# Optimization experiments

Measured on AMD Instinct MI355X. Metric: run time of the kernel, lower is better.

Reference implementation:

```python
import jax, jax.numpy as jnp
import numpy as np

GROUPS = 32
EPS = 1e-5
NUM_HEADS = 16


def group_norm(x, gamma, beta):
    # x: [b, c, s]; GroupNorm over (c//G, s) per group, affine per channel
    b, c, s = x.shape
    xg = x.reshape(b, GROUPS, (c // GROUPS) * s)
    mean = xg.mean(axis=-1, keepdims=True)
    var = xg.var(axis=-1, keepdims=True)
    xn = ((xg - mean) * jax.lax.rsqrt(var + EPS)).reshape(b, c, s)
    return xn * gamma[None, :, None] + beta[None, :, None]


def setup_inputs() -> dict:
    key = jax.random.key(0)
    ks = jax.random.split(key, 8)
    b, c, H, W = 16, 1024, 32, 32
    ctx_dim, Sk = 2048, 256
    x = jax.random.normal(ks[0], (b, c, H, W), jnp.float32)
    context = jax.random.normal(ks[1], (b, Sk, ctx_dim), jnp.float32)
    mask = jax.random.randint(ks[2], (b, Sk), 0, 2, jnp.int32)
    gamma_x = jnp.ones((c,), jnp.float32)
    beta_x = jnp.zeros((c,), jnp.float32)
    gamma_c = jnp.ones((ctx_dim,), jnp.float32)
    beta_c = jnp.zeros((ctx_dim,), jnp.float32)
    Wq = jax.random.normal(ks[3], (c, c), jnp.float32) * (1.0 / np.sqrt(c))
    bq = jnp.zeros((c,), jnp.float32)
    Wkv = jax.random.normal(ks[4], (2 * c, ctx_dim), jnp.float32) * (1.0 / np.sqrt(ctx_dim))
    bkv = jnp.zeros((2 * c,), jnp.float32)
    # proj_out is zero-initialized in the original (zero_module); use small random
    # weights so the attention path contributes to the output / gradients.
    Wp = jax.random.normal(ks[5], (c, c), jnp.float32) * (0.02 / np.sqrt(c))
    bp = jnp.zeros((c,), jnp.float32)
    return {"x": x, "context": context, "mask": mask,
            "gamma_x": gamma_x, "beta_x": beta_x, "gamma_c": gamma_c, "beta_c": beta_c,
            "Wq": Wq, "bq": bq, "Wkv": Wkv, "bkv": bkv, "Wp": Wp, "bp": bp}


def reference(x, context, mask, gamma_x, beta_x, gamma_c, beta_c, Wq, bq, Wkv, bkv, Wp, bp):
    b, c = x.shape[0], x.shape[1]
    spatial = x.shape[2:]
    xf = x.reshape(b, c, -1)                       # [b, c, Sq]
    Sq = xf.shape[-1]
    h_heads = NUM_HEADS
    d = c // h_heads

    # q = conv1x1(GroupNorm(x))
    q = jnp.einsum('oc,bcs->bos', Wq, group_norm(xf, gamma_x, beta_x)) + bq[None, :, None]
    # context -> [b, ctx_dim, Sk], GroupNorm, kv conv1x1
    ctx = jnp.transpose(context, (0, 2, 1))
    ctx_n = group_norm(ctx, gamma_c, beta_c)
    kv = jnp.einsum('oc,bcs->bos', Wkv, ctx_n) + bkv[None, :, None]  # [b, 2c, Sk]
    k, v = kv[:, :c], kv[:, c:]

    # QKVStableMaskedAttention: scale q and k each by 1/sqrt(sqrt(d))
    scale = 1.0 / np.sqrt(np.sqrt(d))
    qh = (q * scale).reshape(b, h_heads, d, Sq)
    kh = (k * scale).reshape(b, h_heads, d, -1)
    vh = v.reshape(b, h_heads, d, -1)
    w = jnp.einsum('bhdt,bhds->bhts', qh, kh)      # [b, h, Sq, Sk]
    mbool = mask.astype(bool)[:, None, None, :]
    w = jnp.where(mbool, w, jnp.float32(-1e9))
    w = jax.nn.softmax(w, axis=-1)                 # stable softmax (max-subtracted)
    a = jnp.einsum('bhts,bhds->bhdt', w, vh).reshape(b, c, Sq)

    h_out = jnp.einsum('oc,bcs->bos', Wp, a) + bp[None, :, None]
    return (xf + h_out).reshape(b, c, *spatial)
```

## Files before the change

### kernel.cpp

```cpp
#include <hip/hip_runtime.h>
#include <stdint.h>

#define DEV static __device__ __forceinline__

typedef unsigned short u16;
typedef u16  u16x8 __attribute__((ext_vector_type(8)));
typedef u16  u16x4 __attribute__((ext_vector_type(4)));
typedef float f32x4 __attribute__((ext_vector_type(4)));
typedef short s16x8 __attribute__((ext_vector_type(8)));

#define BB 16
#define CC 1024
#define SS 1024
#define CTX 2048
#define SKK 256
#define NH 16
#define HD 64
#define NG 32
#define ATT_SCALE 0.35355339059327373f

DEV u16 f2bf(float f) {
  uint32_t u = __float_as_uint(f);
  return (u16)((u + 0x7fffu + ((u >> 16) & 1u)) >> 16);
}
DEV s16x8 ld8(const u16* p) { return __builtin_bit_cast(s16x8, *(const u16x8*)p); }
DEV f32x4 zero4() { f32x4 z = {0.f, 0.f, 0.f, 0.f}; return z; }

DEV void gload_lds16(const void* g, const void* l) {
  __builtin_amdgcn_global_load_lds(
      (const __attribute__((address_space(1))) unsigned int*)(uintptr_t)g,
      (__attribute__((address_space(3))) unsigned int*)(uint32_t)(uintptr_t)l,
      16, 0, 0);
}

__global__ __launch_bounds__(256) void prep_misc(const float* __restrict__ Wq,
                                                 const float* __restrict__ Wkv,
                                                 const float* __restrict__ Wp,
                                                 const int* __restrict__ mask,
                                                 u16* __restrict__ wq_bf,
                                                 u16* __restrict__ wkv_bf,
                                                 u16* __restrict__ wp_bf,
                                                 float* __restrict__ mb) {
  const int bid = blockIdx.x, tid = threadIdx.x;
  const float* src; u16* dst; int i;
  if (bid < 1024)      { src = Wq;  dst = wq_bf;  i = bid * 256 + tid; }
  else if (bid < 5120) { src = Wkv; dst = wkv_bf; i = (bid - 1024) * 256 + tid; }
  else if (bid < 6144) { src = Wp;  dst = wp_bf;  i = (bid - 5120) * 256 + tid; }
  else {
    int j = (bid - 6144) * 256 + tid;
    mb[j] = mask[j] ? 0.f : -1e9f;
    return;
  }
  f32x4 v = ((const f32x4*)src)[i];
  u16x4 o; o[0]=f2bf(v[0]); o[1]=f2bf(v[1]); o[2]=f2bf(v[2]); o[3]=f2bf(v[3]);
  ((u16x4*)dst)[i] = o;
}

__global__ __launch_bounds__(256) void gn_stats_all(const float* __restrict__ x,
                                                    const float* __restrict__ ctx,
                                                    float* __restrict__ stx,
                                                    float* __restrict__ stc) {
  const int bid = blockIdx.x, tid = threadIdx.x;
  float s = 0.f, ss = 0.f;
  float* st; int slot; float inv_n;
  if (bid < 512) {
    const int b = bid >> 5, g = bid & 31;
    const float* p = x + ((size_t)b * CC + g * 32) * SS;
    for (int it = 0; it < 32; ++it) {
      f32x4 v = *(const f32x4*)(p + it * 1024 + tid * 4);
      s  += v[0] + v[1] + v[2] + v[3];
      ss += v[0]*v[0] + v[1]*v[1] + v[2]*v[2] + v[3]*v[3];
    }
    st = stx; slot = bid; inv_n = 1.f / 32768.f;
  } else {
    const int bid2 = bid - 512;
    const int b = bid2 >> 5, g = bid2 & 31;
    const float* p = ctx + (size_t)b * SKK * CTX + g * 64;
    const int ch = tid & 63, r0 = tid >> 6;
    for (int it = 0; it < 64; ++it) {
      float v = p[(size_t)(it * 4 + r0) * CTX + ch];
      s += v; ss += v * v;
    }
    st = stc; slot = bid2; inv_n = 1.f / 16384.f;
  }
  __shared__ float red[512];
  red[tid] = s; red[256 + tid] = ss;
  __syncthreads();
  for (int o = 128; o > 0; o >>= 1) {
    if (tid < o) { red[tid] += red[tid + o]; red[256 + tid] += red[256 + tid + o]; }
    __syncthreads();
  }
  if (tid == 0) {
    float mean = red[0] * inv_n;
    float var  = red[256] * inv_n - mean * mean;
    st[slot * 2 + 0] = mean;
    st[slot * 2 + 1] = rsqrtf(var + 1e-5f);
  }
}

__global__ __launch_bounds__(256) void gn_apply_all(const float* __restrict__ x,
                                                    const float* __restrict__ ctx,
                                                    const float* __restrict__ stx,
                                                    const float* __restrict__ stc,
                                                    const float* __restrict__ gamma_x,
                                                    const float* __restrict__ beta_x,
                                                    const float* __restrict__ gamma_c,
                                                    const float* __restrict__ beta_c,
                                                    u16* __restrict__ xnT,
                                                    u16* __restrict__ ctxn) {
  __shared__ float t[64][65];
  const int bid = blockIdx.x, tid = threadIdx.x;
  if (bid < 8192) {
    size_t i = ((size_t)bid * 256 + tid) * 4;
    int ch = (int)(i & 2047);
    int bs = (int)(i >> 11);
    int b = bs >> 8;
    int g = ch >> 6;
    float mean = stc[(b * 32 + g) * 2], rstd = stc[(b * 32 + g) * 2 + 1];
    f32x4 v  = *(const f32x4*)(ctx + i);
    f32x4 ga = *(const f32x4*)(gamma_c + ch);
    f32x4 be = *(const f32x4*)(beta_c + ch);
    u16x4 o;
    o[0] = f2bf((v[0] - mean) * rstd * ga[0] + be[0]);
    o[1] = f2bf((v[1] - mean) * rstd * ga[1] + be[1]);
    o[2] = f2bf((v[2] - mean) * rstd * ga[2] + be[2]);
    o[3] = f2bf((v[3] - mean) * rstd * ga[3] + be[3]);
    *(u16x4*)(ctxn + i) = o;
    return;
  }
  const int id2 = bid - 8192;
  const int b = id2 >> 8, c0 = ((id2 >> 4) & 15) * 64, s0 = (id2 & 15) * 64;
  const int j = tid & 63, i0 = tid >> 6;
  for (int it = 0; it < 16; ++it) {
    int i = it * 4 + i0;
    int c = c0 + i;
    int g = c >> 5;
    float mean = stx[(b * 32 + g) * 2], rstd = stx[(b * 32 + g) * 2 + 1];
    float v = x[((size_t)b * CC + c) * SS + s0 + j];
    t[i][j] = (v - mean) * rstd * gamma_x[c] + beta_x[c];
  }
  __syncthreads();
  for (int it = 0; it < 16; ++it) {
    int jj = it * 4 + i0;
    xnT[((size_t)b * SS + s0 + jj) * CC + c0 + j] = f2bf(t[j][jj]);
  }
}

DEV void gemm_core(const u16* __restrict__ Ab, const u16* __restrict__ Bb,
                   int K, int ld, u16* lds, f32x4 acc[4][4], int wid, int lane) {
  const int wm = wid >> 1, wn = wid & 1;
  const int fr = lane & 15, hi = lane >> 4;
  const int r0 = lane >> 2, c4 = lane & 3;
  const int sc = (c4 ^ (r0 & 3)) << 3;

  auto STAGE = [&](u16* buf, int kt) {
#pragma unroll
    for (int i = 0; i < 2; ++i) {
      int ch = wid + i * 4;
      long rbase = (long)(ch * 16 + r0);
      gload_lds16(Ab + rbase * ld + kt + sc, buf + ch * 512);
      gload_lds16(Bb + rbase * ld + kt + sc, buf + 4096 + ch * 512);
    }
  };
  auto COMP = [&](const u16* buf) {
    const int ko = ((hi ^ (fr & 3)) << 3);
    s16x8 af[4], bf[4];
#pragma unroll
    for (int m = 0; m < 4; ++m) af[m] = ld8(buf + (wm * 64 + m * 16 + fr) * 32 + ko);
#pragma unroll
    for (int n = 0; n < 4; ++n) bf[n] = ld8(buf + 4096 + (wn * 64 + n * 16 + fr) * 32 + ko);
#pragma unroll
    for (int m = 0; m < 4; ++m)
#pragma unroll
      for (int n = 0; n < 4; ++n)
        acc[m][n] = __builtin_amdgcn_mfma_f32_16x16x32_bf16(af[m], bf[n], acc[m][n], 0, 0, 0);
  };

  const int nt = K >> 5;
  STAGE(lds, 0);
  __syncthreads();
  for (int t = 0; t < nt; t += 2) {
    STAGE(lds + 8192, (t + 1) << 5);
    COMP(lds);
    __syncthreads();
    if (t + 2 < nt) STAGE(lds, (t + 2) << 5);
    COMP(lds + 8192);
    __syncthreads();
  }
}

__global__ __launch_bounds__(256) void gemm_qkv(
    const u16* __restrict__ xnT, const u16* __restrict__ wq,
    const u16* __restrict__ ctxn, const u16* __restrict__ wkv,
    u16* __restrict__ qt, u16* __restrict__ kvt, u16* __restrict__ v2,
    const float* __restrict__ bq, const float* __restrict__ bkv) {
  __shared__ alignas(16) u16 lds[2 * 8192];
  const int tid = threadIdx.x, wid = tid >> 6, lane = tid & 63;
  const int xcd = blockIdx.x & 7, l = blockIdx.x >> 3;
  const bool isQ = l < 128;
  const u16 *Ab, *Bb; const float* bias;
  int K, ld, bx, by, bz;
  if (isQ) {
    int q = xcd * 128 + l;
    bz = q >> 6; int r = q & 63; by = r >> 3; bx = r & 7;
    Ab = xnT + (long)bz * SS * CC + (long)bx * 128 * CC;
    Bb = wq + (long)by * 128 * CC;
    bias = bq; K = CC; ld = CC;
  } else {
    int k = xcd * 64 + (l - 128);
    bz = k >> 5; int r = k & 31; by = r >> 1; bx = r & 1;
    Ab = ctxn + (long)bz * SKK * CTX + (long)bx * 128 * CTX;
    Bb = wkv + (long)by * 128 * CTX;
    bias = bkv; K = CTX; ld = CTX;
  }
  f32x4 acc[4][4];
#pragma unroll
  for (int m = 0; m < 4; ++m)
#pragma unroll
    for (int n = 0; n < 4; ++n) acc[m][n] = zero4();

  gemm_core(Ab, Bb, K, ld, lds, acc, wid, lane);

  const int wm = wid >> 1, wn = wid & 1;
  const int fr = lane & 15, hi = lane >> 4;
  const int rowb = bx * 128 + wm * 64 + hi * 4;
  const int colb = by * 128 + wn * 64 + fr;

  if (isQ) {
    u16* C = qt + (long)bz * SS * CC;
#pragma unroll
    for (int m = 0; m < 4; ++m)
#pragma unroll
      for (int n = 0; n < 4; ++n) {
        int col = colb + n * 16;
        float bia = bias[col];
        f32x4 vv = acc[m][n];
#pragma unroll
        for (int i = 0; i < 4; ++i)
          C[(long)(rowb + m * 16 + i) * CC + col] = f2bf((vv[i] + bia) * ATT_SCALE);
      }
  } else if (by < 8) {
    u16* C = kvt + (long)bz * SKK * CTX;
#pragma unroll
    for (int m = 0; m < 4; ++m)
#pragma unroll
      for (int n = 0; n < 4; ++n) {
        int col = colb + n * 16;
        float bia = bias[col];
        f32x4 vv = acc[m][n];
#pragma unroll
        for (int i = 0; i < 4; ++i)
          C[(long)(rowb + m * 16 + i) * CTX + col] = f2bf((vv[i] + bia) * ATT_SCALE);
      }
  } else {
    u16* V = v2 + (long)bz * CC * SKK;
#pragma unroll
    for (int m = 0; m < 4; ++m)
#pragma unroll
      for (int n = 0; n < 4; ++n) {
        int col = colb + n * 16;
        float bia = bias[col];
        f32x4 vv = acc[m][n];
        u16x4 pk;
#pragma unroll
        for (int i = 0; i < 4; ++i) pk[i] = f2bf(vv[i] + bia);
        *(u16x4*)(V + (long)(col - CC) * SKK + rowb + m * 16) = pk;
      }
  }
}

__global__ __launch_bounds__(256) void gemm_proj(
    const u16* __restrict__ wp, const u16* __restrict__ at,
    float* __restrict__ out, const float* __restrict__ bp,
    const float* __restrict__ x) {
  __shared__ alignas(16) u16 lds[2 * 8192];
  const int tid = threadIdx.x, wid = tid >> 6, lane = tid & 63;
  const int orig = blockIdx.x;
  const int v = (orig & 7) * 128 + (orig >> 3);
  const int bz = v >> 6, r = v & 63, by = r >> 3, bx = r & 7;
  const u16* Ab = wp + (long)bx * 128 * CC;
  const u16* Bb = at + (long)bz * SS * CC + (long)by * 128 * CC;
  f32x4 acc[4][4];
#pragma unroll
  for (int m = 0; m < 4; ++m)
#pragma unroll
    for (int n = 0; n < 4; ++n) acc[m][n] = zero4();

  gemm_core(Ab, Bb, CC, CC, lds, acc, wid, lane);

  float* C = out + (long)bz * SS * CC;
  const float* R = x + (long)bz * SS * CC;
  const int wm = wid >> 1, wn = wid & 1;
  const int fr = lane & 15, hi = lane >> 4;
  const int rowb = bx * 128 + wm * 64 + hi * 4;
  const int colb = by * 128 + wn * 64 + fr;
#pragma unroll
  for (int m = 0; m < 4; ++m) {
#pragma unroll
    for (int n = 0; n < 4; ++n) {
      int col = colb + n * 16;
      f32x4 vv = acc[m][n];
#pragma unroll
      for (int i = 0; i < 4; ++i) {
        int row = rowb + m * 16 + i;
        long idx = (long)row * CC + col;
        C[idx] = R[idx] + vv[i] + bp[row];
      }
    }
  }
}

__global__ __launch_bounds__(256) void attn_fused(const u16* __restrict__ qt,
                                                  const u16* __restrict__ kvt,
                                                  const u16* __restrict__ v2,
                                                  const float* __restrict__ mbias,
                                                  u16* __restrict__ at) {
  __shared__ alignas(16) u16 k_lds[256 * 64];
  __shared__ alignas(16) u16 v_lds[64 * 256];
  const int orig = blockIdx.x + 16 * blockIdx.y + 256 * blockIdx.z;
  const int v = (orig & 7) * 512 + (orig >> 3);
  const int bb = v >> 8, h = (v >> 4) & 15, t0 = (v & 15) * 64;

  const int tid = threadIdx.x, wid = tid >> 6, lane = tid & 63;
  const int fr = lane & 15, hi = lane >> 4;
  const int sw = fr & 7;

#pragma unroll
  for (int it = 0; it < 8; ++it) {
    int lin = (wid * 8 + it) * 1024 + lane * 16;
    int kr = lin >> 7, kc = (lin >> 4) & 7;
    gload_lds16(kvt + ((long)bb * SKK + kr) * CTX + h * HD + ((kc ^ (kr & 7)) << 3),
                (const char*)k_lds + (wid * 8 + it) * 1024);
    int vr = lin >> 9, vc = (lin >> 4) & 31;
    gload_lds16(v2 + ((long)bb * CC + h * HD + vr) * SKK + ((vc ^ (vr & 7)) << 3),
                (const char*)v_lds + (wid * 8 + it) * 1024);
  }

  const u16* qp = qt + ((long)bb * SS + t0 + wid * 16 + fr) * CC + h * HD + hi * 8;
  s16x8 aq0 = ld8(qp), aq1 = ld8(qp + 32);

  __syncthreads();

  f32x4 sc[16];
#pragma unroll
  for (int nf = 0; nf < 16; ++nf) {
    const u16* krow = k_lds + (nf * 16 + fr) * 64;
    s16x8 kb0 = ld8(krow + (((hi) ^ sw) << 3));
    s16x8 kb1 = ld8(krow + (((4 + hi) ^ sw) << 3));
    f32x4 z = zero4();
    z = __builtin_amdgcn_mfma_f32_16x16x32_bf16(aq0, kb0, z, 0, 0, 0);
    sc[nf] = __builtin_amdgcn_mfma_f32_16x16x32_bf16(aq1, kb1, z, 0, 0, 0);
  }

  __syncthreads();

  const float* mb = mbias + bb * SKK + fr;
#pragma unroll
  for (int nf = 0; nf < 16; ++nf) sc[nf] = sc[nf] + mb[nf * 16];

#pragma unroll
  for (int i = 0; i < 4; ++i) {
    float m = sc[0][i];
#pragma unroll
    for (int nf = 1; nf < 16; ++nf) m = fmaxf(m, sc[nf][i]);
#pragma unroll
    for (int d = 1; d < 16; d <<= 1) m = fmaxf(m, __shfl_xor(m, d));
    float s = 0.f;
#pragma unroll
    for (int nf = 0; nf < 16; ++nf) {
      float e = __expf(sc[nf][i] - m);
      sc[nf][i] = e; s += e;
    }
#pragma unroll
    for (int d = 1; d < 16; d <<= 1) s += __shfl_xor(s, d);
    float inv = 1.0f / s;
#pragma unroll
    for (int nf = 0; nf < 16; ++nf) sc[nf][i] *= inv;
  }

  u16* p_base = k_lds + wid * 4096;
#pragma unroll
  for (int nf = 0; nf < 16; ++nf) {
    int c = 2 * nf + (fr >> 3);
#pragma unroll
    for (int i = 0; i < 4; ++i) {
      int t = 4 * hi + i;
      p_base[t * 256 + (((c ^ (t & 7)) << 3)) + sw] = f2bf(sc[nf][i]);
    }
  }

  f32x4 ov[4];
#pragma unroll
  for (int n = 0; n < 4; ++n) ov[n] = zero4();
#pragma unroll
  for (int kk = 0; kk < 8; ++kk) {
    int c = 4 * kk + hi;
    s16x8 pa = ld8(p_base + fr * 256 + ((c ^ sw) << 3));
#pragma unroll
    for (int n = 0; n < 4; ++n) {
      int o = n * 16 + fr;
      s16x8 vb = ld8(v_lds + o * 256 + ((c ^ sw) << 3));
      ov[n] = __builtin_amdgcn_mfma_f32_16x16x32_bf16(pa, vb, ov[n], 0, 0, 0);
    }
  }

  const int rbase = hi * 4;
  u16* po = at + ((long)bb * SS + t0 + wid * 16 + rbase) * CC + h * HD + fr;
#pragma unroll
  for (int n = 0; n < 4; ++n)
#pragma unroll
    for (int i = 0; i < 4; ++i) po[(long)i * CC + n * 16] = f2bf(ov[n][i]);
}

extern "C" void kernel_launch(void* const* d_in, const int* in_sizes, int n_in,
                              void* d_out, int out_size, void* d_ws, size_t ws_size,
                              hipStream_t stream) {
  const float* x       = (const float*)d_in[0];
  const float* context = (const float*)d_in[1];
  const int*   mask    = (const int*)d_in[2];
  const float* gamma_x = (const float*)d_in[3];
  const float* beta_x  = (const float*)d_in[4];
  const float* gamma_c = (const float*)d_in[5];
  const float* beta_c  = (const float*)d_in[6];
  const float* Wq      = (const float*)d_in[7];
  const float* bq      = (const float*)d_in[8];
  const float* Wkv     = (const float*)d_in[9];
  const float* bkv     = (const float*)d_in[10];
  const float* Wp      = (const float*)d_in[11];
  const float* bp      = (const float*)d_in[12];
  float* out = (float*)d_out;

  char* w = (char*)d_ws;
  size_t off = 0;
  u16* wq_bf  = (u16*)(w + off); off += (size_t)CC * CC * 2;
  u16* wkv_bf = (u16*)(w + off); off += (size_t)CTX * CTX * 2;
  u16* wp_bf  = (u16*)(w + off); off += (size_t)CC * CC * 2;
  u16* xnT    = (u16*)(w + off); off += (size_t)BB * SS * CC * 2;
  u16* ctxn   = (u16*)(w + off); off += (size_t)BB * SKK * CTX * 2;
  u16* qt     = (u16*)(w + off); off += (size_t)BB * SS * CC * 2;
  u16* kvt    = (u16*)(w + off); off += (size_t)BB * SKK * CTX * 2;
  u16* v2     = (u16*)(w + off); off += (size_t)BB * CC * SKK * 2;
  u16* at     = (u16*)(w + off); off += (size_t)BB * SS * CC * 2;
  float* mb   = (float*)(w + off); off += (size_t)BB * SKK * 4;
  float* stx  = (float*)(w + off); off += (size_t)BB * NG * 2 * 4;
  float* stc  = (float*)(w + off); off += (size_t)BB * NG * 2 * 4;
  (void)ws_size; (void)in_sizes; (void)n_in; (void)out_size;

  prep_misc<<<6160, 256, 0, stream>>>(Wq, Wkv, Wp, mask, wq_bf, wkv_bf, wp_bf, mb);

  gn_stats_all<<<1024, 256, 0, stream>>>(x, context, stx, stc);

  gn_apply_all<<<12288, 256, 0, stream>>>(x, context, stx, stc,
                                          gamma_x, beta_x, gamma_c, beta_c,
                                          xnT, ctxn);

  gemm_qkv<<<1536, 256, 0, stream>>>(xnT, wq_bf, ctxn, wkv_bf, qt, kvt, v2, bq, bkv);

  attn_fused<<<dim3(16, NH, BB), 256, 0, stream>>>(qt, kvt, v2, mb, at);

  gemm_proj<<<1024, 256, 0, stream>>>(wp_bf, at, out, bp, x);
}
```

Baseline: 413.6 us.

## Switch QKV and projection GEMMs to 256x256 tiles with 4-stage LDS pipeline

Replaces the 128x128, 4-wave double-buffered GEMM core with a 256x256-tile, 8-wave core that keeps a 4-deep ring of LDS stages and waits with explicit vmcnt counters. MFMA issue runs at raised priority. The larger tile raises arithmetic intensity and cuts global reloads, and the deeper pipeline is meant to hide load latency. In exchange it uses 128KB LDS and a 32-tile accumulator per wave, which lowers occupancy. Grids shrink to 384 and 256 blocks, which may leave CUs idle on a 256-CU part.

After: 389.9 us. -5.7%, faster.

```diff
diff --git a/kernel.cpp b/kernel.cpp
--- a/kernel.cpp
+++ b/kernel.cpp
@@ -146,156 +146,155 @@
   }
 }
 
-DEV void gemm_core(const u16* __restrict__ Ab, const u16* __restrict__ Bb,
-                   int K, int ld, u16* lds, f32x4 acc[4][4], int wid, int lane) {
-  const int wm = wid >> 1, wn = wid & 1;
+DEV void gemm8_core(const u16* __restrict__ A, const u16* __restrict__ B,
+                    int ld, int nu, u16* lds, f32x4 acc[8][4], int tid) {
+  const int wid = tid >> 6, lane = tid & 63;
+  const int wr = wid >> 2, wc = wid & 3;
   const int fr = lane & 15, hi = lane >> 4;
-  const int r0 = lane >> 2, c4 = lane & 3;
-  const int sc = (c4 ^ (r0 & 3)) << 3;
-
-  auto STAGE = [&](u16* buf, int kt) {
-#pragma unroll
-    for (int i = 0; i < 2; ++i) {
-      int ch = wid + i * 4;
-      long rbase = (long)(ch * 16 + r0);
-      gload_lds16(Ab + rbase * ld + kt + sc, buf + ch * 512);
-      gload_lds16(Bb + rbase * ld + kt + sc, buf + 4096 + ch * 512);
-    }
+  const int rj0 = tid >> 2, kk = (tid & 3) * 8;
+
+  auto STAGE = [&](int u) {
+    int uc = u < nu ? u : nu - 1;
+    int kof = (uc >> 1) * 64 + (uc & 1) * 32 + kk;
+    u16* la = lds + (u & 3) * 16384;
+    gload_lds16(A + (long)rj0 * ld + kof,         la + tid * 8);
+    gload_lds16(A + (long)(rj0 + 128) * ld + kof, la + 4096 + tid * 8);
+    gload_lds16(B + (long)rj0 * ld + kof,         la + 8192 + tid * 8);
+    gload_lds16(B + (long)(rj0 + 128) * ld + kof, la + 12288 + tid * 8);
   };
-  auto COMP = [&](const u16* buf) {
-    const int ko = ((hi ^ (fr & 3)) << 3);
-    s16x8 af[4], bf[4];
-#pragma unroll
-    for (int m = 0; m < 4; ++m) af[m] = ld8(buf + (wm * 64 + m * 16 + fr) * 32 + ko);
-#pragma unroll
-    for (int n = 0; n < 4; ++n) bf[n] = ld8(buf + 4096 + (wn * 64 + n * 16 + fr) * 32 + ko);
-#pragma unroll
-    for (int m = 0; m < 4; ++m)
+
+  STAGE(0); STAGE(1); STAGE(2);
+
+#pragma unroll 1
+  for (int g = 0; g < nu; ++g) {
+    asm volatile("s_waitcnt vmcnt(8)" ::: "memory");
+    __builtin_amdgcn_s_barrier();
+    __builtin_amdgcn_sched_barrier(0);
+    const u16* As = lds + (g & 3) * 16384;
+    const u16* Bs = As + 8192;
+    s16x8 a[8], b[4];
+#pragma unroll
+    for (int m = 0; m < 8; ++m) a[m] = ld8(As + (wr * 128 + m * 16 + fr) * 32 + hi * 8);
+#pragma unroll
+    for (int n = 0; n < 4; ++n) b[n] = ld8(Bs + (wc * 64 + n * 16 + fr) * 32 + hi * 8);
+    STAGE(g + 3);
+    __builtin_amdgcn_s_setprio(1);
+#pragma unroll
+    for (int m = 0; m < 8; ++m)
 #pragma unroll
       for (int n = 0; n < 4; ++n)
-        acc[m][n] = __builtin_amdgcn_mfma_f32_16x16x32_bf16(af[m], bf[n], acc[m][n], 0, 0, 0);
-  };
-
-  const int nt = K >> 5;
-  STAGE(lds, 0);
-  __syncthreads();
-  for (int t = 0; t < nt; t += 2) {
-    STAGE(lds + 8192, (t + 1) << 5);
-    COMP(lds);
-    __syncthreads();
-    if (t + 2 < nt) STAGE(lds, (t + 2) << 5);
-    COMP(lds + 8192);
-    __syncthreads();
-  }
-}
-
-__global__ __launch_bounds__(256) void gemm_qkv(
+        acc[m][n] = __builtin_amdgcn_mfma_f32_16x16x32_bf16(a[m], b[n], acc[m][n], 0, 0, 0);
+    __builtin_amdgcn_s_setprio(0);
+  }
+}
+
+__global__ __launch_bounds__(512) void gemm_qkv8(
     const u16* __restrict__ xnT, const u16* __restrict__ wq,
     const u16* __restrict__ ctxn, const u16* __restrict__ wkv,
     u16* __restrict__ qt, u16* __restrict__ kvt, u16* __restrict__ v2,
     const float* __restrict__ bq, const float* __restrict__ bkv) {
-  __shared__ alignas(16) u16 lds[2 * 8192];
-  const int tid = threadIdx.x, wid = tid >> 6, lane = tid & 63;
+  __shared__ alignas(16) u16 lds[65536];
+  const int tid = threadIdx.x;
   const int xcd = blockIdx.x & 7, l = blockIdx.x >> 3;
-  const bool isQ = l < 128;
-  const u16 *Ab, *Bb; const float* bias;
-  int K, ld, bx, by, bz;
-  if (isQ) {
-    int q = xcd * 128 + l;
-    bz = q >> 6; int r = q & 63; by = r >> 3; bx = r & 7;
-    Ab = xnT + (long)bz * SS * CC + (long)bx * 128 * CC;
-    Bb = wq + (long)by * 128 * CC;
-    bias = bq; K = CC; ld = CC;
+  const int wid = tid >> 6, lane = tid & 63;
+  const int wr = wid >> 2, wc = wid & 3;
+  const int fr = lane & 15, hi = lane >> 4;
+
+  f32x4 acc[8][4];
+#pragma unroll
+  for (int m = 0; m < 8; ++m)
+#pragma unroll
+    for (int n = 0; n < 4; ++n) acc[m][n] = zero4();
+
+  if (l < 16) {
+    const int kvid = xcd * 16 + l;
+    const int bz = kvid >> 3, tn = kvid & 7;
+    const u16* A = ctxn + (long)bz * SKK * CTX;
+    const u16* B = wkv + (long)tn * 256 * CTX;
+    gemm8_core(A, B, CTX, 64, lds, acc, tid);
+
+    const int rowb = wr * 128 + hi * 4;
+    const int colb = tn * 256 + wc * 64 + fr;
+    if (tn < 4) {
+      u16* C = kvt + (long)bz * SKK * CTX;
+#pragma unroll
+      for (int m = 0; m < 8; ++m)
+#pragma unroll
+        for (int n = 0; n < 4; ++n) {
+          int col = colb + n * 16;
+          float bia = bkv[col];
+          f32x4 vv = acc[m][n];
+#pragma unroll
+          for (int i = 0; i < 4; ++i)
+            C[(long)(rowb + m * 16 + i) * CTX + col] = f2bf((vv[i] + bia) * ATT_SCALE);
+        }
+    } else {
+      u16* V = v2 + (long)bz * CC * SKK;
+#pragma unroll
+      for (int m = 0; m < 8; ++m)
+#pragma unroll
+        for (int n = 0; n < 4; ++n) {
+          int col = colb + n * 16;
+          float bia = bkv[col];
+          f32x4 vv = acc[m][n];
+          u16x4 pk;
+#pragma unroll
+          for (int i = 0; i < 4; ++i) pk[i] = f2bf(vv[i] + bia);
+          *(u16x4*)(V + (long)(col - CC) * SKK + rowb + m * 16) = pk;
+        }
+    }
   } else {
-    int k = xcd * 64 + (l - 128);
-    bz = k >> 5; int r = k & 31; by = r >> 1; bx = r & 1;
-    Ab = ctxn + (long)bz * SKK * CTX + (long)bx * 128 * CTX;
-    Bb = wkv + (long)by * 128 * CTX;
-    bias = bkv; K = CTX; ld = CTX;
-  }
-  f32x4 acc[4][4];
-#pragma unroll
-  for (int m = 0; m < 4; ++m)
-#pragma unroll
-    for (int n = 0; n < 4; ++n) acc[m][n] = zero4();
-
-  gemm_core(Ab, Bb, K, ld, lds, acc, wid, lane);
-
-  const int wm = wid >> 1, wn = wid & 1;
-  const int fr = lane & 15, hi = lane >> 4;
-  const int rowb = bx * 128 + wm * 64 + hi * 4;
-  const int colb = by * 128 + wn * 64 + fr;
-
-  if (isQ) {
+    const int q = xcd * 32 + (l - 16);
+    const int bz = q >> 4, tm = (q >> 2) & 3, tn = q & 3;
+    const u16* A = xnT + (long)bz * SS * CC + (long)tm * 256 * CC;
+    const u16* B = wq + (long)tn * 256 * CC;
+    gemm8_core(A, B, CC, 32, lds, acc, tid);
+
     u16* C = qt + (long)bz * SS * CC;
-#pragma unroll
-    for (int m = 0; m < 4; ++m)
+    const int rowb = tm * 256 + wr * 128 + hi * 4;
+    const int colb = tn * 256 + wc * 64 + fr;
+#pragma unroll
+    for (int m = 0; m < 8; ++m)
 #pragma unroll
       for (int n = 0; n < 4; ++n) {
         int col = colb + n * 16;
-        float bia = bias[col];
+        float bia = bq[col];
         f32x4 vv = acc[m][n];
 #pragma unroll
         for (int i = 0; i < 4; ++i)
           C[(long)(rowb + m * 16 + i) * CC + col] = f2bf((vv[i] + bia) * ATT_SCALE);
       }
-  } else if (by < 8) {
-    u16* C = kvt + (long)bz * SKK * CTX;
-#pragma unroll
-    for (int m = 0; m < 4; ++m)
-#pragma unroll
-      for (int n = 0; n < 4; ++n) {
-        int col = colb + n * 16;
-        float bia = bias[col];
-        f32x4 vv = acc[m][n];
-#pragma unroll
-        for (int i = 0; i < 4; ++i)
-          C[(long)(rowb + m * 16 + i) * CTX + col] = f2bf((vv[i] + bia) * ATT_SCALE);
-      }
-  } else {
-    u16* V = v2 + (long)bz * CC * SKK;
-#pragma unroll
-    for (int m = 0; m < 4; ++m)
-#pragma unroll
-      for (int n = 0; n < 4; ++n) {
-        int col = colb + n * 16;
-        float bia = bias[col];
-        f32x4 vv = acc[m][n];
-        u16x4 pk;
-#pragma unroll
-        for (int i = 0; i < 4; ++i) pk[i] = f2bf(vv[i] + bia);
-        *(u16x4*)(V + (long)(col - CC) * SKK + rowb + m * 16) = pk;
-      }
-  }
-}
-
-__global__ __launch_bounds__(256) void gemm_proj(
+  }
+}
+
+__global__ __launch_bounds__(512) void gemm_proj8(
     const u16* __restrict__ wp, const u16* __restrict__ at,
     float* __restrict__ out, const float* __restrict__ bp,
     const float* __restrict__ x) {
-  __shared__ alignas(16) u16 lds[2 * 8192];
-  const int tid = threadIdx.x, wid = tid >> 6, lane = tid & 63;
-  const int orig = blockIdx.x;
-  const int v = (orig & 7) * 128 + (orig >> 3);
-  const int bz = v >> 6, r = v & 63, by = r >> 3, bx = r & 7;
-  const u16* Ab = wp + (long)bx * 128 * CC;
-  const u16* Bb = at + (long)bz * SS * CC + (long)by * 128 * CC;
-  f32x4 acc[4][4];
-#pragma unroll
-  for (int m = 0; m < 4; ++m)
+  __shared__ alignas(16) u16 lds[65536];
+  const int tid = threadIdx.x;
+  const int v = (blockIdx.x & 7) * 32 + (blockIdx.x >> 3);
+  const int bz = v >> 4, tm = (v >> 2) & 3, tn = v & 3;
+  const int wid = tid >> 6, lane = tid & 63;
+  const int wr = wid >> 2, wc = wid & 3;
+  const int fr = lane & 15, hi = lane >> 4;
+
+  f32x4 acc[8][4];
+#pragma unroll
+  for (int m = 0; m < 8; ++m)
 #pragma unroll
     for (int n = 0; n < 4; ++n) acc[m][n] = zero4();
 
-  gemm_core(Ab, Bb, CC, CC, lds, acc, wid, lane);
-
-  float* C = out + (long)bz * SS * CC;
-  const float* R = x + (long)bz * SS * CC;
-  const int wm = wid >> 1, wn = wid & 1;
-  const int fr = lane & 15, hi = lane >> 4;
-  const int rowb = bx * 128 + wm * 64 + hi * 4;
-  const int colb = by * 128 + wn * 64 + fr;
-#pragma unroll
-  for (int m = 0; m < 4; ++m) {
+  const u16* A = wp + (long)tm * 256 * CC;
+  const u16* B = at + (long)bz * SS * CC + (long)tn * 256 * CC;
+  gemm8_core(A, B, CC, 32, lds, acc, tid);
+
+  float* C = out + (long)bz * CC * SS;
+  const float* R = x + (long)bz * CC * SS;
+  const int rowb = tm * 256 + wr * 128 + hi * 4;
+  const int colb = tn * 256 + wc * 64 + fr;
+#pragma unroll
+  for (int m = 0; m < 8; ++m)
 #pragma unroll
     for (int n = 0; n < 4; ++n) {
       int col = colb + n * 16;
@@ -303,11 +302,10 @@
 #pragma unroll
       for (int i = 0; i < 4; ++i) {
         int row = rowb + m * 16 + i;
-        long idx = (long)row * CC + col;
+        long idx = (long)row * SS + col;
         C[idx] = R[idx] + vv[i] + bp[row];
       }
     }
-  }
 }
 
 __global__ __launch_bounds__(256) void attn_fused(const u16* __restrict__ qt,
@@ -454,9 +452,9 @@
                                           gamma_x, beta_x, gamma_c, beta_c,
                                           xnT, ctxn);
 
-  gemm_qkv<<<1536, 256, 0, stream>>>(xnT, wq_bf, ctxn, wkv_bf, qt, kvt, v2, bq, bkv);
+  gemm_qkv8<<<384, 512, 0, stream>>>(xnT, wq_bf, ctxn, wkv_bf, qt, kvt, v2, bq, bkv);
 
   attn_fused<<<dim3(16, NH, BB), 256, 0, stream>>>(qt, kvt, v2, mb, at);
 
-  gemm_proj<<<1024, 256, 0, stream>>>(wp_bf, at, out, bp, x);
-}
+  gemm_proj8<<<256, 512, 0, stream>>>(wp_bf, at, out, bp, x);
+}
```
